# Kernel optimization log

Measured on AMD Instinct MI355X. Metric: run time of the kernel, lower is better.

The kernel has to match this reference:

```python
import jax, jax.numpy as jnp
import numpy as np

D = 1024      # d_model
H = 16        # nhead
DH = D // H   # head_dim = 64
ROT = DH // 2 # rotary_ndims = 32
FFN = 4096    # d_ffn
B, T, M, N = 4, 1024, 128, 64


def _layernorm(x, g, b, eps=1e-5):
    mu = jnp.mean(x, axis=-1, keepdims=True)
    var = jnp.mean(jnp.square(x - mu), axis=-1, keepdims=True)
    return (x - mu) * jax.lax.rsqrt(var + eps) * g + b


def _rotate_half(x):
    x1, x2 = x[..., : x.shape[-1] // 2], x[..., x.shape[-1] // 2:]
    return jnp.concatenate([-x2, x1], axis=-1)


def setup_inputs() -> dict:
    key = jax.random.key(0)
    ks = jax.random.split(key, 16)
    s = 0.02
    inp = {
        'x': jax.random.normal(ks[0], (B, T, D), jnp.float32),
        'memory': jax.random.normal(ks[1], (B, M, D), jnp.float32),
        'nmr': jax.random.normal(ks[2], (B, N, D), jnp.float32),
        'Wq': jax.random.normal(ks[3], (D, D), jnp.float32) * s,
        'bq': jnp.zeros((D,), jnp.float32),
        'Wk': jax.random.normal(ks[4], (D, D), jnp.float32) * s,
        'bk': jnp.zeros((D,), jnp.float32),
        'Wv': jax.random.normal(ks[5], (D, D), jnp.float32) * s,
        'bv': jnp.zeros((D,), jnp.float32),
        'Wo': jax.random.normal(ks[6], (D, D), jnp.float32) * s,
        'bo': jnp.zeros((D,), jnp.float32),
        'W1': jax.random.normal(ks[7], (D, FFN), jnp.float32) * s,
        'b1': jnp.zeros((FFN,), jnp.float32),
        'W2': jax.random.normal(ks[8], (FFN, D), jnp.float32) * s,
        'b2': jnp.zeros((D,), jnp.float32),
        'ln1_g': jnp.ones((D,), jnp.float32),
        'ln1_b': jnp.zeros((D,), jnp.float32),
        'ln2_g': jnp.ones((D,), jnp.float32),
        'ln2_b': jnp.zeros((D,), jnp.float32),
    }
    return inp


def reference(x, memory, nmr, Wq, bq, Wk, bk, Wv, bv, Wo, bo, W1, b1, W2, b2,
              ln1_g, ln1_b, ln2_g, ln2_b):
    b, t, _ = x.shape
    m, n = memory.shape[1], nmr.shape[1]
    pref = m + n
    L = pref + t

    x_full = jnp.concatenate([memory, nmr, x], axis=1)  # (B, L, D)
    xa = _layernorm(x_full, ln1_g, ln1_b)

    def heads(w, bias):
        return (xa @ w + bias).reshape(b, L, H, DH).transpose(0, 2, 1, 3)  # (B,H,L,DH)

    q = heads(Wq, bq)
    k = heads(Wk, bk)
    v = heads(Wv, bv)

    # partial RoPE on first ROT dims of each head
    pos = jnp.arange(L, dtype=jnp.float32)
    inv_freq = 1.0 / (10000.0 ** (jnp.arange(0, ROT, 2, dtype=jnp.float32) / ROT))
    freqs = pos[:, None] * inv_freq[None, :]              # (L, ROT/2)
    emb = jnp.concatenate([freqs, freqs], axis=-1)        # (L, ROT)
    cos, sin = jnp.cos(emb), jnp.sin(emb)
    qr, qp = q[..., :ROT], q[..., ROT:]
    kr, kp = k[..., :ROT], k[..., ROT:]
    qr = qr * cos + _rotate_half(qr) * sin
    kr = kr * cos + _rotate_half(kr) * sin
    q = jnp.concatenate([qr, qp], axis=-1)
    k = jnp.concatenate([kr, kp], axis=-1)

    # block mask: prefix (memory+nmr) fully bidirectional, target causal,
    # target attends to full prefix, prefix does NOT attend to target.
    i = jnp.arange(L)
    allowed = (i[None, :] < pref) | ((i[:, None] >= pref) & (i[None, :] >= pref)
                                     & (i[None, :] <= i[:, None]))  # (L, L)

    scale = 1.0 / jnp.sqrt(jnp.asarray(DH, jnp.float32))
    scores = jnp.einsum('bhqd,bhkd->bhqk', q, k) * scale
    scores = jnp.where(allowed[None, None], scores, jnp.finfo(scores.dtype).min)
    probs = jax.nn.softmax(scores, axis=-1)
    attn = jnp.einsum('bhqk,bhkd->bhqd', probs, v)        # (B,H,L,DH)
    attn = attn.transpose(0, 2, 1, 3).reshape(b, L, D)

    x_full = attn @ Wo + bo + x_full

    xf = _layernorm(x_full, ln2_g, ln2_b)
    xf = jnp.square(jax.nn.relu(xf @ W1 + b1)) @ W2 + b2
    x_full = x_full + xf

    return x_full[:, pref:]
```

## Files before the change

### kernel.cpp

```cpp
#include <hip/hip_runtime.h>
#include <hip/hip_bf16.h>
#include <math.h>

#define D_   1024
#define H_   16
#define DH_  64
#define FFN_ 4096
#define B_   4
#define T_   1024
#define M_   128
#define N_   64
#define PREF 192
#define L_   1216
#define BL_  (B_*L_)
#define BT_  (B_*T_)

typedef __attribute__((ext_vector_type(4))) float f32x4;
typedef __attribute__((ext_vector_type(8))) short bf16x8;
typedef __attribute__((ext_vector_type(8))) unsigned short u16x8;
typedef const __attribute__((address_space(1))) void gvoid_t;
typedef __attribute__((address_space(3))) void lvoid_t;

#define LGKM0 asm volatile("s_waitcnt lgkmcnt(0)" ::: "memory")
#define CFENCE asm volatile("" ::: "memory")

__device__ __forceinline__ void gl_lds16(const void* g, void* l) {
    __builtin_amdgcn_global_load_lds((gvoid_t*)g, (lvoid_t*)l, 16, 0, 0);
}

__device__ __forceinline__ ushort f2bf(float x) {
    union { __hip_bfloat16 h; ushort u; } cv;
    cv.h = __float2bfloat16(x);
    return cv.u;
}

__device__ __forceinline__ u16x8 pack8(float4 a, float4 b) {
    u16x8 r;
    r[0]=f2bf(a.x); r[1]=f2bf(a.y); r[2]=f2bf(a.z); r[3]=f2bf(a.w);
    r[4]=f2bf(b.x); r[5]=f2bf(b.y); r[6]=f2bf(b.z); r[7]=f2bf(b.w);
    return r;
}

__device__ __forceinline__ float block_reduce_sum256(float v, float* sbuf) {
#pragma unroll
    for (int o = 32; o > 0; o >>= 1) v += __shfl_xor(v, o, 64);
    int w = threadIdx.x >> 6;
    if ((threadIdx.x & 63) == 0) sbuf[w] = v;
    __syncthreads();
    float r = sbuf[0] + sbuf[1] + sbuf[2] + sbuf[3];
    __syncthreads();
    return r;
}

__device__ __forceinline__ void wtr_body(const float* __restrict__ W,
                                         ushort* __restrict__ Wt, int K, int Nc)
{
    __shared__ float tl[64][65];
    int c0 = blockIdx.x << 6, k0 = blockIdx.y << 6;
    int tid = threadIdx.x;
    int rr = tid >> 4, c4 = (tid & 15) << 2;
#pragma unroll
    for (int p = 0; p < 4; ++p) {
        int r = (p << 4) + rr;
        float4 v = *(const float4*)(W + (size_t)(k0 + r) * Nc + c0 + c4);
        tl[r][c4+0] = v.x; tl[r][c4+1] = v.y; tl[r][c4+2] = v.z; tl[r][c4+3] = v.w;
    }
    __syncthreads();
#pragma unroll
    for (int p = 0; p < 4; ++p) {
        int rT = (p << 4) + rr;
        ushort4 uv;
        uv.x = f2bf(tl[c4+0][rT]);
        uv.y = f2bf(tl[c4+1][rT]);
        uv.z = f2bf(tl[c4+2][rT]);
        uv.w = f2bf(tl[c4+3][rT]);
        *(ushort4*)(Wt + (size_t)(c0 + rT) * K + k0 + c4) = uv;
    }
}

__global__ __launch_bounds__(256) void wtr_kernel(
    const float* __restrict__ W, ushort* __restrict__ Wt, int K, int Nc)
{ wtr_body(W, Wt, K, Nc); }

__global__ __launch_bounds__(256) void wtr4_kernel(
    const float* __restrict__ W0, const float* __restrict__ W1,
    const float* __restrict__ W2, const float* __restrict__ W3,
    ushort* __restrict__ T0, ushort* __restrict__ T1,
    ushort* __restrict__ T2, ushort* __restrict__ T3)
{
    const float* W; ushort* T;
    switch (blockIdx.z) {
        case 0: W = W0; T = T0; break;
        case 1: W = W1; T = T1; break;
        case 2: W = W2; T = T2; break;
        default: W = W3; T = T3; break;
    }
    wtr_body(W, T, D_, D_);
}

__global__ __launch_bounds__(256) void prep_kernel(
    float* __restrict__ tab, const float* __restrict__ bq,
    const float* __restrict__ bk, const float* __restrict__ bv,
    float* __restrict__ ob)
{
    int i = blockIdx.x * 256 + threadIdx.x;
    if (i < L_ * 32) {
        int pos = i >> 5, idx = i & 31;
        int fi = idx & 15;
        float invf = exp2f(-(float)fi * 0.83048202372f);
        float th = (float)pos * invf;
        tab[i] = (idx < 16) ? cosf(th) : sinf(th);
    } else {
        int j = i - L_ * 32;
        if (j < 3072) {
            float v = (j < 1024) ? bq[j] : (j < 2048 ? bk[j - 1024] : bv[j - 2048]);
            ob[j] = v;
        }
    }
}

__global__ __launch_bounds__(256) void ln1_concat_kernel(
    const float* __restrict__ x, const float* __restrict__ mem,
    const float* __restrict__ nmr, const float* __restrict__ g,
    const float* __restrict__ be, float* __restrict__ x_full,
    ushort* __restrict__ xa_bf)
{
    __shared__ float sbuf[4];
    int row = blockIdx.x;
    int b = row / L_, pos = row % L_;
    const float* src;
    if (pos < M_)          src = mem + ((size_t)b*M_ + pos)      * D_;
    else if (pos < M_+N_)  src = nmr + ((size_t)b*N_ + (pos-M_)) * D_;
    else                   src = x   + ((size_t)b*T_ + (pos-PREF))*D_;

    int c = threadIdx.x << 2;
    float4 v = *(const float4*)(src + c);
    float s = v.x + v.y + v.z + v.w;
    s = block_reduce_sum256(s, sbuf);
    float mu = s * (1.0f / D_);
    float dx = v.x - mu, dy = v.y - mu, dz = v.z - mu, dw = v.w - mu;
    float q = dx*dx + dy*dy + dz*dz + dw*dw;
    q = block_reduce_sum256(q, sbuf);
    float inv = rsqrtf(q * (1.0f / D_) + 1e-5f);
    float4 gv = *(const float4*)(g + c);
    float4 bv = *(const float4*)(be + c);
    ushort4 o;
    o.x = f2bf(dx*inv*gv.x + bv.x);
    o.y = f2bf(dy*inv*gv.y + bv.y);
    o.z = f2bf(dz*inv*gv.z + bv.z);
    o.w = f2bf(dw*inv*gv.w + bv.w);
    *(float4*)(x_full + (size_t)row*D_ + c) = v;
    *(ushort4*)(xa_bf + (size_t)row*D_ + c) = o;
}

__global__ __launch_bounds__(256) void ln2_kernel(
    const float* __restrict__ src, const float* __restrict__ g,
    const float* __restrict__ be, ushort* __restrict__ dst)
{
    __shared__ float sbuf[4];
    int row = blockIdx.x;
    int c = threadIdx.x << 2;
    float4 v = *(const float4*)(src + (size_t)row*D_ + c);
    float s = v.x + v.y + v.z + v.w;
    s = block_reduce_sum256(s, sbuf);
    float mu = s * (1.0f / D_);
    float dx = v.x - mu, dy = v.y - mu, dz = v.z - mu, dw = v.w - mu;
    float q = dx*dx + dy*dy + dz*dz + dw*dw;
    q = block_reduce_sum256(q, sbuf);
    float inv = rsqrtf(q * (1.0f / D_) + 1e-5f);
    float4 gv = *(const float4*)(g + c);
    float4 bv = *(const float4*)(be + c);
    ushort4 o;
    o.x = f2bf(dx*inv*gv.x + bv.x);
    o.y = f2bf(dy*inv*gv.y + bv.y);
    o.z = f2bf(dz*inv*gv.z + bv.z);
    o.w = f2bf(dw*inv*gv.w + bv.w);
    *(ushort4*)(dst + (size_t)row*D_ + c) = o;
}

__global__ __launch_bounds__(256) void reduce2_out_kernel(
    const float* __restrict__ part, const float* __restrict__ b2,
    const float* __restrict__ x2, float* __restrict__ out)
{
    int row = blockIdx.x;
    int c = threadIdx.x << 2;
    size_t o = (size_t)row * D_ + c;
    const size_t S = (size_t)BT_ * D_;
    float4 p0 = *(const float4*)(part + o);
    float4 p1 = *(const float4*)(part + S + o);
    float4 bb = *(const float4*)(b2 + c);
    float4 rv = *(const float4*)(x2 + o);
    float4 v;
    v.x = p0.x + p1.x + bb.x + rv.x;
    v.y = p0.y + p1.y + bb.y + rv.y;
    v.z = p0.z + p1.z + bb.z + rv.z;
    v.w = p0.w + p1.w + bb.w + rv.w;
    *(float4*)(out + o) = v;
}

__global__ __launch_bounds__(256) void gemm_bf16_kernel(
    const ushort* __restrict__ A, const ushort* __restrict__ Bt,
    const float* __restrict__ bias, const float* __restrict__ rtab,
    void* __restrict__ Cout, int Nc, int Kstride, int Klen, int mode)
{
    __shared__ ushort SM[24576];
    char* SMb = (char*)SM;
    int tid = threadIdx.x;
    int lane = tid & 63, w = tid >> 6;
    int wm = w >> 1, wn = w & 1;
    int nx = gridDim.x;
    int flat = blockIdx.y * nx + blockIdx.x;
    int cpx = (nx * gridDim.y) >> 3;
    int sz = (flat & 7) * cpx + (flat >> 3);
    int row0 = (sz / nx) << 7, col0 = (sz % nx) << 7;
    int l15 = lane & 15, l4 = lane >> 4;

    f32x4 acc[4][4] = {};

    int r_a = tid >> 2;
    int sc  = tid & 3;
    int lcOff = (sc ^ ((r_a >> 1) & 3)) << 3;
    const ushort* Arow  = A  + (size_t)(row0 + r_a)      * Kstride;
    const ushort* Arow2 = A  + (size_t)(row0 + 64 + r_a) * Kstride;
    const ushort* Brow  = Bt + (size_t)(col0 + r_a)      * Kstride;
    const ushort* Brow2 = Bt + (size_t)(col0 + 64 + r_a) * Kstride;

#define STAGEQ(bb, k0rel)                                                    \
    do { char* Ab = SMb + (bb)*8192; char* Bb = SMb + 24576 + (bb)*8192;     \
        gl_lds16(Arow  + (k0rel) + lcOff, Ab + (tid << 4));                  \
        gl_lds16(Arow2 + (k0rel) + lcOff, Ab + 4096 + (tid << 4));           \
        gl_lds16(Brow  + (k0rel) + lcOff, Bb + (tid << 4));                  \
        gl_lds16(Brow2 + (k0rel) + lcOff, Bb + 4096 + (tid << 4));           \
    } while (0)

    int nIt = Klen >> 5;
    STAGEQ(0, 0);
    STAGEQ(1, 32);
    int cur = 0;
    for (int it = 0; it < nIt; ++it) {
        if (it + 1 < nIt) {
            asm volatile("s_waitcnt vmcnt(4)" ::: "memory");
        } else {
            asm volatile("s_waitcnt vmcnt(0)" ::: "memory");
        }
        __builtin_amdgcn_s_barrier();
        CFENCE;
        if (it + 2 < nIt) {
            int s2 = cur + 2; if (s2 >= 3) s2 -= 3;
            STAGEQ(s2, (it + 2) << 5);
        }
        const ushort* As = (const ushort*)(SMb + cur*8192);
        const ushort* Bs = (const ushort*)(SMb + 24576 + cur*8192);
        bf16x8 af[4], bfr[4];
#pragma unroll
        for (int i = 0; i < 4; ++i) {
            int ra = (wm << 6) + (i << 4) + l15;
            af[i]  = *(const bf16x8*)(&As[ra*32 + ((l4 ^ ((ra >> 1) & 3)) << 3)]);
            int rb = (wn << 6) + (i << 4) + l15;
            bfr[i] = *(const bf16x8*)(&Bs[rb*32 + ((l4 ^ ((rb >> 1) & 3)) << 3)]);
        }
#pragma unroll
        for (int i = 0; i < 4; ++i)
#pragma unroll
            for (int j = 0; j < 4; ++j)
                acc[i][j] = __builtin_amdgcn_mfma_f32_16x16x32_bf16(af[i], bfr[j], acc[i][j], 0, 0, 0);
        CFENCE;
        cur = (cur + 1 == 3) ? 0 : cur + 1;
    }
#undef STAGEQ
    __syncthreads();

    float bcol[4];
#pragma unroll
    for (int j = 0; j < 4; ++j) bcol[j] = bias[col0 + (wn << 6) + (j << 4) + l15];

    float* scr = (float*)SM + w * 1088;
    int rr = lane >> 2, cseg = lane & 3;
    int hh = ((col0 & 1023) + (wn << 6)) >> 6;
    int which = col0 >> 10;

#pragma unroll
    for (int i = 0; i < 4; ++i) {
        LGKM0;
#pragma unroll
        for (int j = 0; j < 4; ++j)
#pragma unroll
            for (int r = 0; r < 4; ++r)
                scr[((l4 << 2) + r)*68 + (j << 4) + l15] = acc[i][j][r] + bcol[j];
        LGKM0;
        int grow = row0 + (wm << 6) + (i << 4) + rr;

        if (which == 2) {
            int r0g = row0 + (wm << 6) + (i << 4);
            int bb = r0g / L_;
            int posb = r0g - bb * L_;
            float4 v0, v1, v2, v3;
            v0.x = scr[ 0*68 + lane]; v0.y = scr[ 1*68 + lane];
            v0.z = scr[ 2*68 + lane]; v0.w = scr[ 3*68 + lane];
            v1.x = scr[ 4*68 + lane]; v1.y = scr[ 5*68 + lane];
            v1.z = scr[ 6*68 + lane]; v1.w = scr[ 7*68 + lane];
            v2.x = scr[ 8*68 + lane]; v2.y = scr[ 9*68 + lane];
            v2.z = scr[10*68 + lane]; v2.w = scr[11*68 + lane];
            v3.x = scr[12*68 + lane]; v3.y = scr[13*68 + lane];
            v3.z = scr[14*68 + lane]; v3.w = scr[15*68 + lane];
            ushort* O = (ushort*)Cout + 2*(size_t)BL_*D_;
            size_t base = ((size_t)(bb*H_ + hh)*64 + lane)*L_ + posb;
            *(u16x8*)(O + base)     = pack8(v0, v1);
            *(u16x8*)(O + base + 8) = pack8(v2, v3);
        } else {
            int bb = grow / L_;
            int pos = grow - bb * L_;
            float4 a0 = *(float4*)&scr[rr*68 + (cseg << 4) + 0];
            float4 a1 = *(float4*)&scr[rr*68 + (cseg << 4) + 4];
            float4 a2 = *(float4*)&scr[rr*68 + (cseg << 4) + 8];
            float4 a3 = *(float4*)&scr[rr*68 + (cseg << 4) + 12];
            if (cseg < 2) {
                int oseg = cseg ^ 1;
                float4 p0 = *(float4*)&scr[rr*68 + (oseg << 4) + 0];
                float4 p1 = *(float4*)&scr[rr*68 + (oseg << 4) + 4];
                float4 p2 = *(float4*)&scr[rr*68 + (oseg << 4) + 8];
                float4 p3 = *(float4*)&scr[rr*68 + (oseg << 4) + 12];
                const float* tb = rtab + pos*32;
                float4 c0 = *(const float4*)(tb + 0),  c1 = *(const float4*)(tb + 4);
                float4 c2 = *(const float4*)(tb + 8),  c3 = *(const float4*)(tb + 12);
                float4 s0 = *(const float4*)(tb + 16), s1 = *(const float4*)(tb + 20);
                float4 s2 = *(const float4*)(tb + 24), s3 = *(const float4*)(tb + 28);
                float sg = (cseg == 0) ? -1.f : 1.f;
                a0.x = a0.x*c0.x + sg*p0.x*s0.x; a0.y = a0.y*c0.y + sg*p0.y*s0.y;
                a0.z = a0.z*c0.z + sg*p0.z*s0.z; a0.w = a0.w*c0.w + sg*p0.w*s0.w;
                a1.x = a1.x*c1.x + sg*p1.x*s1.x; a1.y = a1.y*c1.y + sg*p1.y*s1.y;
                a1.z = a1.z*c1.z + sg*p1.z*s1.z; a1.w = a1.w*c1.w + sg*p1.w*s1.w;
                a2.x = a2.x*c2.x + sg*p2.x*s2.x; a2.y = a2.y*c2.y + sg*p2.y*s2.y;
                a2.z = a2.z*c2.z + sg*p2.z*s2.z; a2.w = a2.w*c2.w + sg*p2.w*s2.w;
                a3.x = a3.x*c3.x + sg*p3.x*s3.x; a3.y = a3.y*c3.y + sg*p3.y*s3.y;
                a3.z = a3.z*c3.z + sg*p3.z*s3.z; a3.w = a3.w*c3.w + sg*p3.w*s3.w;
            }
            ushort* O = (ushort*)Cout + (size_t)which * ((size_t)BL_*D_);
            size_t base = (((size_t)(bb*H_ + hh)*L_ + pos) << 6) + (cseg << 4);
            *(u16x8*)(O + base)     = pack8(a0, a1);
            *(u16x8*)(O + base + 8) = pack8(a2, a3);
        }
    }
}

template<int MODE>
__global__ __launch_bounds__(512) void gemm_wide_kernel(
    const ushort* __restrict__ A, const ushort* __restrict__ Bt,
    const float* __restrict__ bias, void* __restrict__ Cout,
    int Nc, int Kstride, int Klen)
{
    __shared__ ushort SM[36864];
    char* SMb = (char*)SM;

    int tid = threadIdx.x;
    int lane = tid & 63, w = tid >> 6;
    int l15 = lane & 15, l4 = lane >> 4;

    int nx = gridDim.x;
    int flat = blockIdx.y * nx + blockIdx.x;
    int cpx = (nx * gridDim.y) >> 3;
    int sz = (flat & 7) * cpx + (flat >> 3);
    int row0 = (sz / nx) << 7, col0 = (sz % nx) << 8;
    int kbase = blockIdx.z * Klen;

    int wm = w >> 2, wn = w & 3;

    f32x4 acc[4][4] = {};

    int rA = tid >> 2, scA = tid & 3;
    int lcA = (scA ^ ((rA >> 1) & 3)) << 3;
    const ushort* Ar = A + (size_t)(row0 + rA) * Kstride + kbase + lcA;
    int lcB1 = (scA ^ (((128 + rA) >> 1) & 3)) << 3;
    const ushort* Br0 = Bt + (size_t)(col0 + rA)       * Kstride + kbase + lcA;
    const ushort* Br1 = Bt + (size_t)(col0 + 128 + rA) * Kstride + kbase + lcB1;

#define STG1(bb, k0rel)                                                       \
    do {                                                                      \
        gl_lds16(Ar  + (k0rel), SMb + (bb)*8192 + (tid << 4));                \
        gl_lds16(Br0 + (k0rel), SMb + 24576 + (bb)*16384 + (tid << 4));       \
        gl_lds16(Br1 + (k0rel), SMb + 24576 + (bb)*16384 + 8192 + (tid << 4));\
    } while (0)

    int nIt = Klen >> 5;
    STG1(0, 0);
    STG1(1, 32);
    int cur = 0;
    for (int it = 0; it < nIt; ++it) {
        if (it + 1 < nIt) {
            asm volatile("s_waitcnt vmcnt(3)" ::: "memory");
        } else {
            asm volatile("s_waitcnt vmcnt(0)" ::: "memory");
        }
        __builtin_amdgcn_s_barrier();
        CFENCE;
        if (it + 2 < nIt) {
            int s2 = cur + 2; if (s2 >= 3) s2 -= 3;
            STG1(s2, (it + 2) << 5);
        }
        const ushort* As = (const ushort*)(SMb + cur*8192);
        const ushort* Bs = (const ushort*)(SMb + 24576 + cur*16384);
        bf16x8 af[4], bfr[4];
#pragma unroll
        for (int i = 0; i < 4; ++i) {
            int ra = (wm << 6) + (i << 4) + l15;
            af[i]  = *(const bf16x8*)(&As[ra*32 + ((l4 ^ ((ra >> 1) & 3)) << 3)]);
            int rb = (wn << 6) + (i << 4) + l15;
            bfr[i] = *(const bf16x8*)(&Bs[rb*32 + ((l4 ^ ((rb >> 1) & 3)) << 3)]);
        }
#pragma unroll
        for (int i = 0; i < 4; ++i)
#pragma unroll
            for (int j = 0; j < 4; ++j)
                acc[i][j] = __builtin_amdgcn_mfma_f32_16x16x32_bf16(af[i], bfr[j], acc[i][j], 0, 0, 0);
        CFENCE;
        cur = (cur + 1 == 3) ? 0 : cur + 1;
    }
#undef STG1
    __syncthreads();

    float bcol[4] = {0.f, 0.f, 0.f, 0.f};
    if (MODE != 4) {
#pragma unroll
        for (int j = 0; j < 4; ++j) bcol[j] = bias[col0 + (wn << 6) + (j << 4) + l15];
    }

    float* scr = (float*)SMb + w * 1088;
    int rr = lane >> 2, cseg = lane & 3;
    int colbase = col0 + (wn << 6);

#pragma unroll
    for (int i = 0; i < 4; ++i) {
        LGKM0;
#pragma unroll
        for (int j = 0; j < 4; ++j)
#pragma unroll
            for (int r = 0; r < 4; ++r) {
                float v = acc[i][j][r] + bcol[j];
                if (MODE == 3) { v = fmaxf(v, 0.f); v *= v; }
                scr[((l4 << 2) + r)*68 + (j << 4) + l15] = v;
            }
        LGKM0;
        int grow = row0 + (wm << 6) + (i << 4) + rr;
        float4 q0 = *(float4*)&scr[rr*68 + (cseg << 4) + 0];
        float4 q1 = *(float4*)&scr[rr*68 + (cseg << 4) + 4];
        float4 q2 = *(float4*)&scr[rr*68 + (cseg << 4) + 8];
        float4 q3 = *(float4*)&scr[rr*68 + (cseg << 4) + 12];
        int gcol = colbase + (cseg << 4);
        if (MODE == 3) {
            ushort* O = (ushort*)Cout;
            *(u16x8*)(O + (size_t)grow*Nc + gcol)     = pack8(q0, q1);
            *(u16x8*)(O + (size_t)grow*Nc + gcol + 8) = pack8(q2, q3);
        } else {
            float* O = (float*)Cout + (size_t)blockIdx.z * ((size_t)BT_ * D_);
            size_t o = (size_t)grow*Nc + gcol;
            *(float4*)(O + o)      = q0;
            *(float4*)(O + o + 4)  = q1;
            *(float4*)(O + o + 8)  = q2;
            *(float4*)(O + o + 12) = q3;
        }
    }
}

__global__ __launch_bounds__(256) void gemm_sk2_kernel(
    const ushort* __restrict__ A, const ushort* __restrict__ Bt,
    const float* __restrict__ bias, const float* __restrict__ res,
    float* __restrict__ Cout, int Nc, int Kstride, int Klen, int mode)
{
    __shared__ ushort SM[36864];
    char* SMb = (char*)SM;
    int tid = threadIdx.x;
    int lane = tid & 63, w = tid >> 6;
    int l15 = lane & 15, l4 = lane >> 4;
    int g = w >> 1, wm = w & 1;

    int nx = gridDim.x;
    int flat = blockIdx.y * nx + blockIdx.x;
    int cpx = (nx * gridDim.y) >> 3;
    int sz = (flat & 7) * cpx + (flat >> 3);
    int row0 = (sz / nx) << 7, col0 = (sz % nx) << 6;

    f32x4 acc[4][4] = {};
    const int kl = Klen >> 1;
    const int kb = g * kl;

    int gt = tid & 127;
    int rB = gt >> 2, sc = gt & 3;
    const ushort* Abase = A  + (size_t)row0 * Kstride + kb;
    const ushort* Bbase = Bt + (size_t)col0 * Kstride + kb;
    char* ALg = SMb + g * 24576;
    char* BLg = SMb + 49152 + g * 12288;

#define STG2(bb, k0rel)                                                       \
    do {                                                                      \
        _Pragma("unroll")                                                     \
        for (int p = 0; p < 4; ++p) {                                         \
            int rw = (p << 5) + rB; int lc = sc ^ ((rw >> 1) & 3);            \
            gl_lds16(Abase + (size_t)rw*Kstride + (k0rel) + (lc << 3),        \
                     ALg + (bb)*8192 + (p << 11) + (gt << 4));                \
        }                                                                     \
        _Pragma("unroll")                                                     \
        for (int p = 0; p < 2; ++p) {                                         \
            int rw = (p << 5) + rB; int lc = sc ^ ((rw >> 1) & 3);            \
            gl_lds16(Bbase + (size_t)rw*Kstride + (k0rel) + (lc << 3),        \
                     BLg + (bb)*4096 + (p << 11) + (gt << 4));                \
        }                                                                     \
    } while (0)

    int nIt = kl >> 5;
    STG2(0, 0);
    STG2(1, 32);
    int cur = 0;
    for (int it = 0; it < nIt; ++it) {
        if (it + 1 < nIt) {
            asm volatile("s_waitcnt vmcnt(6)" ::: "memory");
        } else {
            asm volatile("s_waitcnt vmcnt(0)" ::: "memory");
        }
        __builtin_amdgcn_s_barrier();
        CFENCE;
        if (it + 2 < nIt) {
            int s2 = cur + 2; if (s2 >= 3) s2 -= 3;
            STG2(s2, (it + 2) << 5);
        }
        const ushort* As = (const ushort*)(ALg + cur*8192);
        const ushort* Bs = (const ushort*)(BLg + cur*4096);
        bf16x8 af[4], bfr[4];
#pragma unroll
        for (int i = 0; i < 4; ++i) {
            int ra = (wm << 6) + (i << 4) + l15;
            af[i]  = *(const bf16x8*)(&As[ra*32 + ((l4 ^ ((ra >> 1) & 3)) << 3)]);
            int rb = (i << 4) + l15;
            bfr[i] = *(const bf16x8*)(&Bs[rb*32 + ((l4 ^ ((rb >> 1) & 3)) << 3)]);
        }
#pragma unroll
        for (int i = 0; i < 4; ++i)
#pragma unroll
            for (int j = 0; j < 4; ++j)
                acc[i][j] = __builtin_amdgcn_mfma_f32_16x16x32_bf16(af[i], bfr[j], acc[i][j], 0, 0, 0);
        CFENCE;
        cur = (cur + 1 == 3) ? 0 : cur + 1;
    }
#undef STG2
    __syncthreads();

    float* scr2 = (float*)SMb;
    if (g == 1) {
#pragma unroll
        for (int i = 0; i < 4; ++i)
#pragma unroll
            for (int j = 0; j < 4; ++j)
#pragma unroll
                for (int r = 0; r < 4; ++r)
                    scr2[((wm << 6) + (i << 4) + (l4 << 2) + r)*68 + (j << 4) + l15] = acc[i][j][r];
    }
    __syncthreads();
    if (g == 1) return;
#pragma unroll
    for (int i = 0; i < 4; ++i)
#pragma unroll
        for (int j = 0; j < 4; ++j)
#pragma unroll
            for (int r = 0; r < 4; ++r)
                acc[i][j][r] += scr2[((wm << 6) + (i << 4) + (l4 << 2) + r)*68 + (j << 4) + l15];

    float bcol[4];
#pragma unroll
    for (int j = 0; j < 4; ++j) bcol[j] = bias[col0 + (j << 4) + l15];
    int rr = lane >> 2, cseg = lane & 3;
    float* scr = (float*)(SMb + 36864) + w * 1088;

#pragma unroll
    for (int i = 0; i < 4; ++i) {
        LGKM0;
#pragma unroll
        for (int j = 0; j < 4; ++j)
#pragma unroll
            for (int r = 0; r < 4; ++r)
                scr[((l4 << 2) + r)*68 + (j << 4) + l15] = acc[i][j][r] + bcol[j];
        LGKM0;
        int grow = row0 + (wm << 6) + (i << 4) + rr;
        float4 q0 = *(float4*)&scr[rr*68 + (cseg << 4) + 0];
        float4 q1 = *(float4*)&scr[rr*68 + (cseg << 4) + 4];
        float4 q2 = *(float4*)&scr[rr*68 + (cseg << 4) + 8];
        float4 q3 = *(float4*)&scr[rr*68 + (cseg << 4) + 12];
        int gcol = col0 + (cseg << 4);
        size_t roff;
        if (mode == 2) {
            int rs = (grow >> 10)*L_ + PREF + (grow & (T_-1));
            roff = (size_t)rs*D_ + gcol;
        } else {
            roff = (size_t)grow*Nc + gcol;
        }
        float4 r0 = *(const float4*)(res + roff);
        float4 r1 = *(const float4*)(res + roff + 4);
        float4 r2 = *(const float4*)(res + roff + 8);
        float4 r3 = *(const float4*)(res + roff + 12);
        q0.x += r0.x; q0.y += r0.y; q0.z += r0.z; q0.w += r0.w;
        q1.x += r1.x; q1.y += r1.y; q1.z += r1.z; q1.w += r1.w;
        q2.x += r2.x; q2.y += r2.y; q2.z += r2.z; q2.w += r2.w;
        q3.x += r3.x; q3.y += r3.y; q3.z += r3.z; q3.w += r3.w;
        size_t o = (size_t)grow*Nc + gcol;
        *(float4*)(Cout + o)      = q0;
        *(float4*)(Cout + o + 4)  = q1;
        *(float4*)(Cout + o + 8)  = q2;
        *(float4*)(Cout + o + 12) = q3;
    }
}

__global__ __launch_bounds__(256) void attn_mfma_kernel(
    const ushort* __restrict__ qhd, const ushort* __restrict__ khd,
    const ushort* __restrict__ vt, ushort* __restrict__ attn_bf)
{
    __shared__ ushort Ks[2][64*64];
    __shared__ ushort Vs[2][64*64];
    __shared__ ushort Ps[4*16*64];

    int bid0 = blockIdx.x;
    int bid = (bid0 & 7) * (gridDim.x >> 3) + (bid0 >> 3);
    int p  = bid & 7;
    int h  = (bid >> 3) & (H_ - 1);
    int b  = bid >> 7;
    int tid = threadIdx.x, lane = tid & 63, w = tid >> 6;
    int l15 = lane & 15, lg = lane >> 4;
    int wq0 = w << 4;
    size_t bh = (size_t)(b * H_ + h);

    int srow = tid >> 3;
    int sslot = tid & 7;
    ushort* Ps_w = Ps + (w << 10);
    const float SC = 0.125f * 1.4426950408889634f;

#define STAGE_T(buf, t)                                                     \
    do { int j0s = (t) << 6;                                                \
        gl_lds16(khd + (bh * L_ + j0s + srow) * 64 + ((sslot ^ (srow & 7)) << 3),      \
                 (char*)Ks[buf] + (tid << 4));                              \
        gl_lds16(khd + (bh * L_ + j0s + 32 + srow) * 64 + ((sslot ^ ((32+srow) & 7)) << 3), \
                 (char*)Ks[buf] + ((256 + tid) << 4));                      \
        gl_lds16(vt + (bh * 64 + srow) * L_ + j0s + ((sslot ^ (srow & 7)) << 3),       \
                 (char*)Vs[buf] + (tid << 4));                              \
        gl_lds16(vt + (bh * 64 + 32 + srow) * L_ + j0s + ((sslot ^ ((32+srow) & 7)) << 3), \
                 (char*)Vs[buf] + ((256 + tid) << 4));                      \
    } while (0)

#pragma unroll
    for (int sub = 0; sub < 2; ++sub) {
        int qb = sub ? p : (15 - p);
        int i0 = PREF + (qb << 6);
        const ushort* qrow = qhd + (bh * L_ + i0 + wq0 + l15) * 64;
        bf16x8 bq0 = *(const bf16x8*)(qrow + (lg << 3));
        bf16x8 bq1 = *(const bf16x8*)(qrow + 32 + (lg << 3));

        f32x4 acc[4] = {};
        float mrun = -INFINITY;
        float lsum = 0.f;
        int qcap = i0 + wq0 + l15;

        int ntile = 4 + qb;
        STAGE_T(0, 0);
        __syncthreads();
        int cur = 0;
        for (int t = 0; t < ntile; ++t) {
            if (t + 1 < ntile) STAGE_T(cur ^ 1, t + 1);
            const ushort* Kc = Ks[cur];
            const ushort* Vc = Vs[cur];

            f32x4 s4[4];
            __builtin_amdgcn_s_setprio(1);
#pragma unroll
            for (int st = 0; st < 4; ++st) {
                int rk = (st << 4) + l15;
                bf16x8 ak0 = *(const bf16x8*)(Kc + (rk << 6) + ((lg       ^ (rk & 7)) << 3));
                bf16x8 ak1 = *(const bf16x8*)(Kc + (rk << 6) + (((4 + lg) ^ (rk & 7)) << 3));
                f32x4 z = {};
                z = __builtin_amdgcn_mfma_f32_16x16x32_bf16(ak0, bq0, z, 0, 0, 0);
                z = __builtin_amdgcn_mfma_f32_16x16x32_bf16(ak1, bq1, z, 0, 0, 0);
                s4[st] = z;
            }
            __builtin_amdgcn_s_setprio(0);

            int j0 = t << 6;
            float sv[4][4];
            bool diag = (t == ntile - 1);
            int kbq = j0 + (lg << 2);
#pragma unroll
            for (int st = 0; st < 4; ++st)
#pragma unroll
                for (int r = 0; r < 4; ++r) {
                    float s = s4[st][r] * SC;
                    if (diag && (kbq + (st << 4) + r > qcap)) s = -INFINITY;
                    sv[st][r] = s;
                }
            float bm;
            {
                float t0 = fmaxf(fmaxf(sv[0][0], sv[0][1]), fmaxf(sv[0][2], sv[0][3]));
                float t1 = fmaxf(fmaxf(sv[1][0], sv[1][1]), fmaxf(sv[1][2], sv[1][3]));
                float t2 = fmaxf(fmaxf(sv[2][0], sv[2][1]), fmaxf(sv[2][2], sv[2][3]));
                float t3 = fmaxf(fmaxf(sv[3][0], sv[3][1]), fmaxf(sv[3][2], sv[3][3]));
                bm = fmaxf(fmaxf(t0, t1), fmaxf(t2, t3));
            }
            bm = fmaxf(bm, __shfl_xor(bm, 16, 64));
            bm = fmaxf(bm, __shfl_xor(bm, 32, 64));

            float mn = fmaxf(mrun, bm);
            float cr = exp2f(mrun - mn);
            mrun = mn;
            float pe[4][4];
            float ps = 0.f;
#pragma unroll
            for (int st = 0; st < 4; ++st)
#pragma unroll
                for (int r = 0; r < 4; ++r) {
                    float e = exp2f(sv[st][r] - mn);
                    pe[st][r] = e; ps += e;
                }
            ps += __shfl_xor(ps, 16, 64);
            ps += __shfl_xor(ps, 32, 64);
            lsum = lsum * cr + ps;
#pragma unroll
            for (int su = 0; su < 4; ++su) acc[su] *= cr;

#pragma unroll
            for (int st = 0; st < 4; ++st) {
                int slot = (st << 1) + (lg >> 1);
                int sb = ((lg & 1) << 3);
#pragma unroll
                for (int rp = 0; rp < 2; ++rp) {
                    uint u = (uint)f2bf(pe[st][2*rp]) | ((uint)f2bf(pe[st][2*rp+1]) << 16);
                    *(uint*)((char*)Ps_w + l15*128 + ((slot ^ (l15 & 7)) << 4) + sb + (rp << 2)) = u;
                }
            }
            {
                bf16x8 bp0 = *(const bf16x8*)((char*)Ps_w + l15*128 + ((lg       ^ (l15 & 7)) << 4));
                bf16x8 bp1 = *(const bf16x8*)((char*)Ps_w + l15*128 + (((4 + lg) ^ (l15 & 7)) << 4));
                __builtin_amdgcn_s_setprio(1);
#pragma unroll
                for (int su = 0; su < 4; ++su) {
                    int rd = (su << 4) + l15;
                    bf16x8 av0 = *(const bf16x8*)(Vc + (rd << 6) + ((lg       ^ (rd & 7)) << 3));
                    bf16x8 av1 = *(const bf16x8*)(Vc + (rd << 6) + (((4 + lg) ^ (rd & 7)) << 3));
                    acc[su] = __builtin_amdgcn_mfma_f32_16x16x32_bf16(av0, bp0, acc[su], 0, 0, 0);
                    acc[su] = __builtin_amdgcn_mfma_f32_16x16x32_bf16(av1, bp1, acc[su], 0, 0, 0);
                }
                __builtin_amdgcn_s_setprio(0);
            }
            __syncthreads();
            cur ^= 1;
        }

        float rl = 1.0f / lsum;
        size_t orow = (size_t)b * T_ + (i0 - PREF) + wq0 + l15;
#pragma unroll
        for (int su = 0; su < 4; ++su) {
            ushort4 o4;
            o4.x = f2bf(acc[su][0] * rl);
            o4.y = f2bf(acc[su][1] * rl);
            o4.z = f2bf(acc[su][2] * rl);
            o4.w = f2bf(acc[su][3] * rl);
            *(ushort4*)(attn_bf + orow * D_ + (h << 6) + (su << 4) + (lg << 2)) = o4;
        }
        __syncthreads();
    }
#undef STAGE_T
}

extern "C" void kernel_launch(void* const* d_in, const int* in_sizes, int n_in,
                              void* d_out, int out_size, void* d_ws, size_t ws_size,
                              hipStream_t stream) {
    const float* x   = (const float*)d_in[0];
    const float* mem = (const float*)d_in[1];
    const float* nmr = (const float*)d_in[2];
    const float* Wq  = (const float*)d_in[3];
    const float* bq  = (const float*)d_in[4];
    const float* Wk  = (const float*)d_in[5];
    const float* bk  = (const float*)d_in[6];
    const float* Wv  = (const float*)d_in[7];
    const float* bv  = (const float*)d_in[8];
    const float* Wo  = (const float*)d_in[9];
    const float* bo  = (const float*)d_in[10];
    const float* W1  = (const float*)d_in[11];
    const float* b1  = (const float*)d_in[12];
    const float* W2  = (const float*)d_in[13];
    const float* b2  = (const float*)d_in[14];
    const float* g1  = (const float*)d_in[15];
    const float* be1 = (const float*)d_in[16];
    const float* g2  = (const float*)d_in[17];
    const float* be2 = (const float*)d_in[18];
    float* out = (float*)d_out;

    const size_t BLD = (size_t)BL_ * D_;
    const size_t BTD = (size_t)BT_ * D_;

    float* f = (float*)d_ws;
    float* x_full = f;
    float* x2     = f + BLD;
    float* bqkv   = x2 + BTD;
    float* rtab   = bqkv + 4096;
    ushort* bfb   = (ushort*)(rtab + (size_t)L_*32);
    ushort* xa_bf   = bfb;
    ushort* qhd     = bfb + BLD;
    ushort* khd     = bfb + 2*BLD;
    ushort* vt      = bfb + 3*BLD;
    ushort* h1_bf   = bfb + 4*BLD;
    ushort* wq_bf = h1_bf + (size_t)BT_*FFN_;
    ushort* wk_bf = wq_bf + (size_t)D_*D_;
    ushort* wv_bf = wk_bf + (size_t)D_*D_;
    ushort* wo_bf = wv_bf + (size_t)D_*D_;
    ushort* w1_bf = wo_bf + (size_t)D_*D_;
    ushort* w2_bf = w1_bf + (size_t)D_*FFN_;
    float* partials = (float*)(w2_bf + (size_t)FFN_*D_);
    ushort* attn_bf = xa_bf;
    ushort* ln2_bf  = qhd;

    wtr4_kernel<<<dim3(16, 16, 4), 256, 0, stream>>>(Wq, Wk, Wv, Wo,
                                                     wq_bf, wk_bf, wv_bf, wo_bf);
    wtr_kernel<<<dim3(FFN_/64, D_/64),   256, 0, stream>>>(W1, w1_bf, D_,   FFN_);
    wtr_kernel<<<dim3(D_/64,   FFN_/64), 256, 0, stream>>>(W2, w2_bf, FFN_, D_);
    prep_kernel<<<(L_*32 + 3072 + 255)/256, 256, 0, stream>>>(rtab, bq, bk, bv, bqkv);

    ln1_concat_kernel<<<BL_, 256, 0, stream>>>(x, mem, nmr, g1, be1, x_full, xa_bf);

    gemm_bf16_kernel<<<dim3(3072/128, BL_/128), 256, 0, stream>>>(
        xa_bf, wq_bf, bqkv, rtab, qhd, D_, D_, D_, 7);

    attn_mfma_kernel<<<B_*H_*8, 256, 0, stream>>>(qhd, khd, vt, attn_bf);

    gemm_sk2_kernel<<<dim3(D_/64, BT_/128), 256, 0, stream>>>(
        attn_bf, wo_bf, bo, x_full, x2, D_, D_, D_, 2);

    ln2_kernel<<<BT_, 256, 0, stream>>>(x2, g2, be2, ln2_bf);

    gemm_wide_kernel<3><<<dim3(FFN_/256, BT_/128), 512, 0, stream>>>(
        ln2_bf, w1_bf, b1, h1_bf, FFN_, D_, D_);

    gemm_wide_kernel<4><<<dim3(D_/256, BT_/128, 2), 512, 0, stream>>>(
        h1_bf, w2_bf, nullptr, partials, D_, FFN_, FFN_/2);
    reduce2_out_kernel<<<BT_, 256, 0, stream>>>(partials, b2, x2, out);
}
```

Before: 232.7 us.

## Use wide split-K GEMM for Wo projection and fuse reduction into LN2

The output projection now uses the generic wide GEMM kernel (MODE 4) with a 2-way K split writing fp32 partials, instead of the dedicated in-block split-K kernel with a fused bias/residual epilogue. The partial sum, bias, residual add from x_full and layernorm 2 are folded into one new row kernel that writes both x2 and the bf16 LN2 output. This removes the old ln2 pass re-reading x2 and reuses the presumably better-tuned wide GEMM. In exchange it adds an extra fp32 partials write and read round trip through global memory.

```diff
diff --git a/kernel.cpp b/kernel.cpp
--- a/kernel.cpp
+++ b/kernel.cpp
@@ -153,14 +153,28 @@
     *(ushort4*)(xa_bf + (size_t)row*D_ + c) = o;
 }
 
-__global__ __launch_bounds__(256) void ln2_kernel(
-    const float* __restrict__ src, const float* __restrict__ g,
-    const float* __restrict__ be, ushort* __restrict__ dst)
+__global__ __launch_bounds__(256) void reduce2_ln2_kernel(
+    const float* __restrict__ part, const float* __restrict__ bo,
+    const float* __restrict__ x_full, const float* __restrict__ g,
+    const float* __restrict__ be, float* __restrict__ x2,
+    ushort* __restrict__ ln2_bf)
 {
     __shared__ float sbuf[4];
     int row = blockIdx.x;
     int c = threadIdx.x << 2;
-    float4 v = *(const float4*)(src + (size_t)row*D_ + c);
+    size_t o = (size_t)row * D_ + c;
+    float4 a  = *(const float4*)(part + o);
+    float4 b2 = *(const float4*)(part + (size_t)BT_*D_ + o);
+    float4 bb = *(const float4*)(bo + c);
+    int rr = (row >> 10)*L_ + PREF + (row & (T_-1));
+    float4 rv = *(const float4*)(x_full + (size_t)rr*D_ + c);
+    float4 v;
+    v.x = a.x + b2.x + bb.x + rv.x;
+    v.y = a.y + b2.y + bb.y + rv.y;
+    v.z = a.z + b2.z + bb.z + rv.z;
+    v.w = a.w + b2.w + bb.w + rv.w;
+    *(float4*)(x2 + o) = v;
+
     float s = v.x + v.y + v.z + v.w;
     s = block_reduce_sum256(s, sbuf);
     float mu = s * (1.0f / D_);
@@ -170,12 +184,12 @@
     float inv = rsqrtf(q * (1.0f / D_) + 1e-5f);
     float4 gv = *(const float4*)(g + c);
     float4 bv = *(const float4*)(be + c);
-    ushort4 o;
-    o.x = f2bf(dx*inv*gv.x + bv.x);
-    o.y = f2bf(dy*inv*gv.y + bv.y);
-    o.z = f2bf(dz*inv*gv.z + bv.z);
-    o.w = f2bf(dw*inv*gv.w + bv.w);
-    *(ushort4*)(dst + (size_t)row*D_ + c) = o;
+    ushort4 ov;
+    ov.x = f2bf(dx*inv*gv.x + bv.x);
+    ov.y = f2bf(dy*inv*gv.y + bv.y);
+    ov.z = f2bf(dz*inv*gv.z + bv.z);
+    ov.w = f2bf(dw*inv*gv.w + bv.w);
+    *(ushort4*)(ln2_bf + o) = ov;
 }
 
 __global__ __launch_bounds__(256) void reduce2_out_kernel(
@@ -461,152 +475,6 @@
     }
 }
 
-__global__ __launch_bounds__(256) void gemm_sk2_kernel(
-    const ushort* __restrict__ A, const ushort* __restrict__ Bt,
-    const float* __restrict__ bias, const float* __restrict__ res,
-    float* __restrict__ Cout, int Nc, int Kstride, int Klen, int mode)
-{
-    __shared__ ushort SM[36864];
-    char* SMb = (char*)SM;
-    int tid = threadIdx.x;
-    int lane = tid & 63, w = tid >> 6;
-    int l15 = lane & 15, l4 = lane >> 4;
-    int g = w >> 1, wm = w & 1;
-
-    int nx = gridDim.x;
-    int flat = blockIdx.y * nx + blockIdx.x;
-    int cpx = (nx * gridDim.y) >> 3;
-    int sz = (flat & 7) * cpx + (flat >> 3);
-    int row0 = (sz / nx) << 7, col0 = (sz % nx) << 6;
-
-    f32x4 acc[4][4] = {};
-    const int kl = Klen >> 1;
-    const int kb = g * kl;
-
-    int gt = tid & 127;
-    int rB = gt >> 2, sc = gt & 3;
-    const ushort* Abase = A  + (size_t)row0 * Kstride + kb;
-    const ushort* Bbase = Bt + (size_t)col0 * Kstride + kb;
-    char* ALg = SMb + g * 24576;
-    char* BLg = SMb + 49152 + g * 12288;
-
-#define STG2(bb, k0rel)                                                       \
-    do {                                                                      \
-        _Pragma("unroll")                                                     \
-        for (int p = 0; p < 4; ++p) {                                         \
-            int rw = (p << 5) + rB; int lc = sc ^ ((rw >> 1) & 3);            \
-            gl_lds16(Abase + (size_t)rw*Kstride + (k0rel) + (lc << 3),        \
-                     ALg + (bb)*8192 + (p << 11) + (gt << 4));                \
-        }                                                                     \
-        _Pragma("unroll")                                                     \
-        for (int p = 0; p < 2; ++p) {                                         \
-            int rw = (p << 5) + rB; int lc = sc ^ ((rw >> 1) & 3);            \
-            gl_lds16(Bbase + (size_t)rw*Kstride + (k0rel) + (lc << 3),        \
-                     BLg + (bb)*4096 + (p << 11) + (gt << 4));                \
-        }                                                                     \
-    } while (0)
-
-    int nIt = kl >> 5;
-    STG2(0, 0);
-    STG2(1, 32);
-    int cur = 0;
-    for (int it = 0; it < nIt; ++it) {
-        if (it + 1 < nIt) {
-            asm volatile("s_waitcnt vmcnt(6)" ::: "memory");
-        } else {
-            asm volatile("s_waitcnt vmcnt(0)" ::: "memory");
-        }
-        __builtin_amdgcn_s_barrier();
-        CFENCE;
-        if (it + 2 < nIt) {
-            int s2 = cur + 2; if (s2 >= 3) s2 -= 3;
-            STG2(s2, (it + 2) << 5);
-        }
-        const ushort* As = (const ushort*)(ALg + cur*8192);
-        const ushort* Bs = (const ushort*)(BLg + cur*4096);
-        bf16x8 af[4], bfr[4];
-#pragma unroll
-        for (int i = 0; i < 4; ++i) {
-            int ra = (wm << 6) + (i << 4) + l15;
-            af[i]  = *(const bf16x8*)(&As[ra*32 + ((l4 ^ ((ra >> 1) & 3)) << 3)]);
-            int rb = (i << 4) + l15;
-            bfr[i] = *(const bf16x8*)(&Bs[rb*32 + ((l4 ^ ((rb >> 1) & 3)) << 3)]);
-        }
-#pragma unroll
-        for (int i = 0; i < 4; ++i)
-#pragma unroll
-            for (int j = 0; j < 4; ++j)
-                acc[i][j] = __builtin_amdgcn_mfma_f32_16x16x32_bf16(af[i], bfr[j], acc[i][j], 0, 0, 0);
-        CFENCE;
-        cur = (cur + 1 == 3) ? 0 : cur + 1;
-    }
-#undef STG2
-    __syncthreads();
-
-    float* scr2 = (float*)SMb;
-    if (g == 1) {
-#pragma unroll
-        for (int i = 0; i < 4; ++i)
-#pragma unroll
-            for (int j = 0; j < 4; ++j)
-#pragma unroll
-                for (int r = 0; r < 4; ++r)
-                    scr2[((wm << 6) + (i << 4) + (l4 << 2) + r)*68 + (j << 4) + l15] = acc[i][j][r];
-    }
-    __syncthreads();
-    if (g == 1) return;
-#pragma unroll
-    for (int i = 0; i < 4; ++i)
-#pragma unroll
-        for (int j = 0; j < 4; ++j)
-#pragma unroll
-            for (int r = 0; r < 4; ++r)
-                acc[i][j][r] += scr2[((wm << 6) + (i << 4) + (l4 << 2) + r)*68 + (j << 4) + l15];
-
-    float bcol[4];
-#pragma unroll
-    for (int j = 0; j < 4; ++j) bcol[j] = bias[col0 + (j << 4) + l15];
-    int rr = lane >> 2, cseg = lane & 3;
-    float* scr = (float*)(SMb + 36864) + w * 1088;
-
-#pragma unroll
-    for (int i = 0; i < 4; ++i) {
-        LGKM0;
-#pragma unroll
-        for (int j = 0; j < 4; ++j)
-#pragma unroll
-            for (int r = 0; r < 4; ++r)
-                scr[((l4 << 2) + r)*68 + (j << 4) + l15] = acc[i][j][r] + bcol[j];
-        LGKM0;
-        int grow = row0 + (wm << 6) + (i << 4) + rr;
-        float4 q0 = *(float4*)&scr[rr*68 + (cseg << 4) + 0];
-        float4 q1 = *(float4*)&scr[rr*68 + (cseg << 4) + 4];
-        float4 q2 = *(float4*)&scr[rr*68 + (cseg << 4) + 8];
-        float4 q3 = *(float4*)&scr[rr*68 + (cseg << 4) + 12];
-        int gcol = col0 + (cseg << 4);
-        size_t roff;
-        if (mode == 2) {
-            int rs = (grow >> 10)*L_ + PREF + (grow & (T_-1));
-            roff = (size_t)rs*D_ + gcol;
-        } else {
-            roff = (size_t)grow*Nc + gcol;
-        }
-        float4 r0 = *(const float4*)(res + roff);
-        float4 r1 = *(const float4*)(res + roff + 4);
-        float4 r2 = *(const float4*)(res + roff + 8);
-        float4 r3 = *(const float4*)(res + roff + 12);
-        q0.x += r0.x; q0.y += r0.y; q0.z += r0.z; q0.w += r0.w;
-        q1.x += r1.x; q1.y += r1.y; q1.z += r1.z; q1.w += r1.w;
-        q2.x += r2.x; q2.y += r2.y; q2.z += r2.z; q2.w += r2.w;
-        q3.x += r3.x; q3.y += r3.y; q3.z += r3.z; q3.w += r3.w;
-        size_t o = (size_t)grow*Nc + gcol;
-        *(float4*)(Cout + o)      = q0;
-        *(float4*)(Cout + o + 4)  = q1;
-        *(float4*)(Cout + o + 8)  = q2;
-        *(float4*)(Cout + o + 12) = q3;
-    }
-}
-
 __global__ __launch_bounds__(256) void attn_mfma_kernel(
     const ushort* __restrict__ qhd, const ushort* __restrict__ khd,
     const ushort* __restrict__ vt, ushort* __restrict__ attn_bf)
@@ -824,10 +692,9 @@
 
     attn_mfma_kernel<<<B_*H_*8, 256, 0, stream>>>(qhd, khd, vt, attn_bf);
 
-    gemm_sk2_kernel<<<dim3(D_/64, BT_/128), 256, 0, stream>>>(
-        attn_bf, wo_bf, bo, x_full, x2, D_, D_, D_, 2);
-
-    ln2_kernel<<<BT_, 256, 0, stream>>>(x2, g2, be2, ln2_bf);
+    gemm_wide_kernel<4><<<dim3(D_/256, BT_/128, 2), 512, 0, stream>>>(
+        attn_bf, wo_bf, nullptr, partials, D_, D_, D_/2);
+    reduce2_ln2_kernel<<<BT_, 256, 0, stream>>>(partials, bo, x_full, g2, be2, x2, ln2_bf);
 
     gemm_wide_kernel<3><<<dim3(FFN_/256, BT_/128), 512, 0, stream>>>(
         ln2_bf, w1_bf, b1, h1_bf, FFN_, D_, D_);
```

New measurement: 239.3 us. 1.03x slower.
